# Kernel tuning notes

Hardware: AMD Instinct MI355X
Metric: run time of the kernel (lower is better)

## Reference

```python
import jax, jax.numpy as jnp
import numpy as np
from math import sqrt

NUM_HEADS = 8
HIDDEN = 768
ATTN_DIM = HIDDEN // NUM_HEADS  # 96
NEG = -1e10


def setup_inputs() -> dict:
    key = jax.random.key(0)
    ks = jax.random.split(key, 6)
    b, s, dim = 8, 1024, 768
    scale = 1.0 / sqrt(dim)
    return {
        "span_embeddings": jax.random.normal(ks[0], (b, s, dim), dtype=jnp.float32),
        "span_tags": jax.random.randint(ks[1], (b, s), 0, 5),
        "w_weight": jax.random.normal(ks[2], (1, dim), dtype=jnp.float32) * scale,
        "w_q": jax.random.normal(ks[3], (HIDDEN, dim), dtype=jnp.float32) * scale,
        "w_k": jax.random.normal(ks[4], (HIDDEN, dim), dtype=jnp.float32) * scale,
        "w_v": jax.random.normal(ks[5], (HIDDEN, dim), dtype=jnp.float32) * scale,
    }


def reference(span_embeddings, span_tags, w_weight, w_q, w_k, w_v):
    b, s, _ = span_embeddings.shape
    pad = span_tags == 0  # [b, s]

    # additive span attention weights: Linear(dim -> 1), mask padded, softmax over seq
    attn_weights = span_embeddings @ w_weight.T  # [b, s, 1]
    attn_weights = jnp.where(pad[:, :, None], NEG, attn_weights)
    attn_weights = jax.nn.softmax(attn_weights, axis=1)

    # NOTE: original views hidden as (attn_dim, num_heads) in that order
    qs = (span_embeddings @ w_q.T).reshape(b, s, ATTN_DIM, NUM_HEADS)
    ks = (span_embeddings @ w_k.T).reshape(b, s, ATTN_DIM, NUM_HEADS)
    vs = (span_embeddings @ w_v.T).reshape(b, s, ATTN_DIM, NUM_HEADS)

    rel = jnp.einsum('bqdh,bkdh->bqkh', qs, ks) / sqrt(ATTN_DIM)  # [b,q,k,h]
    # original masks along query axis (relevance_weights[span_tags.eq(0)] = NEG)
    rel = jnp.where(pad[:, :, None, None], NEG, rel)
    # original softmax(dim=-1) -> over the HEADS axis (faithful quirk)
    rel = jax.nn.softmax(rel, axis=-1)

    span_value = jnp.einsum('bqkh,bkdh->bqdh', rel, vs).reshape(b, s, HIDDEN)
    weighted_value = jnp.sum(attn_weights * span_value, axis=1)  # [b, hidden]
    return weighted_value
```

## Files before the change

kernel.cpp:

```cpp
#include <hip/hip_runtime.h>
#include <hip/hip_bf16.h>
#include <math.h>

#define NEGV (-1e10f)

typedef __attribute__((ext_vector_type(8))) short bf16x8;
typedef __attribute__((ext_vector_type(4))) float f32x4;
typedef __attribute__((ext_vector_type(16))) float f32x16;

static __device__ __forceinline__ unsigned short f2bf(float f) {
  unsigned int u = __builtin_bit_cast(unsigned int, f);
  unsigned int r = (u + 0x7fffu + ((u >> 16) & 1u)) >> 16;
  return (unsigned short)r;
}
static __device__ __forceinline__ float bf2f(unsigned short v) {
  return __builtin_bit_cast(float, (unsigned int)v << 16);
}

#define GLD16(g, l)                                                   \
  __builtin_amdgcn_global_load_lds(                                   \
      (const __attribute__((address_space(1))) void*)(g),             \
      (__attribute__((address_space(3))) void*)(l), 16, 0, 0)

__global__ __launch_bounds__(256) void cast_inputs(
    const float* __restrict__ emb, const int* __restrict__ tags,
    const float* __restrict__ ww, const float* __restrict__ wq,
    const float* __restrict__ wk, const float* __restrict__ wv,
    unsigned short* __restrict__ embbf, float* __restrict__ logits,
    unsigned short* __restrict__ wbf) {
  int bx = blockIdx.x;
  if (bx < 2048) {
    int w = threadIdx.x >> 6, lane = threadIdx.x & 63;
    int row = bx * 4 + w;
    const float4* src = (const float4*)(emb + (size_t)row * 768);
    const float4* wsrc = (const float4*)ww;
    ushort4* dst = (ushort4*)(embbf + (size_t)row * 768);
    float d = 0.f;
#pragma unroll
    for (int j = 0; j < 3; j++) {
      int idx = lane + 64 * j;
      float4 v = src[idx];
      float4 wv = wsrc[idx];
      d += v.x * wv.x + v.y * wv.y + v.z * wv.z + v.w * wv.w;
      ushort4 o;
      o.x = f2bf(v.x); o.y = f2bf(v.y); o.z = f2bf(v.z); o.w = f2bf(v.w);
      dst[idx] = o;
    }
#pragma unroll
    for (int off = 32; off; off >>= 1) d += __shfl_xor(d, off);
    if (lane == 0) logits[row] = (tags[row] == 0) ? NEGV : d;
  } else {
    int g = bx - 2048;
    int z = g / 576;
    int idx = (g - z * 576) * 256 + threadIdx.x;
    const float* src = (z == 0) ? wq : (z == 1) ? wk : wv;
    float4 v = ((const float4*)src)[idx];
    ushort4 o;
    o.x = f2bf(v.x); o.y = f2bf(v.y); o.z = f2bf(v.z); o.w = f2bf(v.w);
    ((ushort4*)(wbf + (size_t)z * 589824))[idx] = o;
  }
}

__global__ __launch_bounds__(256) void softmax_aw(
    const float* __restrict__ logits, float* __restrict__ aw) {
  __shared__ float red[4];
  int b = blockIdx.x, t = threadIdx.x;
  const float* L = logits + b * 1024;
  float x0 = L[t], x1 = L[t + 256], x2 = L[t + 512], x3 = L[t + 768];
  float m = fmaxf(fmaxf(x0, x1), fmaxf(x2, x3));
#pragma unroll
  for (int off = 32; off; off >>= 1) m = fmaxf(m, __shfl_xor(m, off));
  if ((t & 63) == 0) red[t >> 6] = m;
  __syncthreads();
  m = fmaxf(fmaxf(red[0], red[1]), fmaxf(red[2], red[3]));
  float e0 = __expf(x0 - m), e1 = __expf(x1 - m), e2 = __expf(x2 - m),
        e3 = __expf(x3 - m);
  float s = e0 + e1 + e2 + e3;
#pragma unroll
  for (int off = 32; off; off >>= 1) s += __shfl_xor(s, off);
  __syncthreads();
  if ((t & 63) == 0) red[t >> 6] = s;
  __syncthreads();
  float inv = 1.0f / (red[0] + red[1] + red[2] + red[3]);
  float* A = aw + b * 1024;
  A[t] = e0 * inv; A[t + 256] = e1 * inv;
  A[t + 512] = e2 * inv; A[t + 768] = e3 * inv;
}

__global__ __launch_bounds__(256) void qkv_gemm(
    const unsigned short* __restrict__ A, const unsigned short* __restrict__ Wbf,
    unsigned short* __restrict__ Qf, unsigned short* __restrict__ Kf,
    unsigned short* __restrict__ Vbf) {
  __shared__ __align__(16) unsigned short sm[16640];
  unsigned short* As = sm;
  unsigned short* Bs = sm + 8192;
  int z = blockIdx.z;
  const unsigned short* B = Wbf + (size_t)z * 589824;
  int mb = blockIdx.x * 128, nb = blockIdx.y * 128;
  int tid = threadIdx.x;
  int w = tid >> 6, lane = tid & 63;
  int wm = w >> 1, wn = w & 1;
  int c = lane & 15, quad = lane >> 4;
  int lrow = lane >> 2;
  int lcol = ((lane & 3) ^ (lrow & 3)) * 8;
  const unsigned short* Ag = A + (size_t)(mb + w * 32 + lrow) * 768 + lcol;
  const unsigned short* Bg = B + (size_t)(nb + w * 32 + lrow) * 768 + lcol;
  int woff = w * 1024;

#define PREFETCH(buf, kb)                                              \
  do {                                                                 \
    GLD16(Ag + (kb), As + (buf) * 4096 + woff);                        \
    GLD16(Ag + (kb) + 16 * 768, As + (buf) * 4096 + woff + 512);       \
    GLD16(Bg + (kb), Bs + (buf) * 4096 + woff);                        \
    GLD16(Bg + (kb) + 16 * 768, Bs + (buf) * 4096 + woff + 512);       \
  } while (0)

  f32x4 acc[4][4];
#pragma unroll
  for (int i = 0; i < 4; i++)
#pragma unroll
    for (int j = 0; j < 4; j++) acc[i][j] = 0;

  PREFETCH(0, 0);
  for (int it = 0; it < 24; it++) {
    __syncthreads();
    if (it + 1 < 24) PREFETCH((it + 1) & 1, (it + 1) * 32);
    const unsigned short* Ab = As + (it & 1) * 4096;
    const unsigned short* Bb = Bs + (it & 1) * 4096;
    int sw = (quad ^ (c & 3)) * 8;
    bf16x8 af[4], bfr[4];
#pragma unroll
    for (int i = 0; i < 4; i++)
      af[i] = *(const bf16x8*)&Ab[(wm * 64 + i * 16 + c) * 32 + sw];
#pragma unroll
    for (int j = 0; j < 4; j++)
      bfr[j] = *(const bf16x8*)&Bb[(wn * 64 + j * 16 + c) * 32 + sw];
#pragma unroll
    for (int i = 0; i < 4; i++)
#pragma unroll
      for (int j = 0; j < 4; j++)
        acc[i][j] = __builtin_amdgcn_mfma_f32_16x16x32_bf16(af[i], bfr[j],
                                                            acc[i][j], 0, 0, 0);
  }
  __syncthreads();

  if (z == 2) {
#pragma unroll
    for (int i = 0; i < 4; i++)
#pragma unroll
      for (int j = 0; j < 4; j++)
#pragma unroll
        for (int r = 0; r < 4; r++) {
          int rowg = mb + wm * 64 + i * 16 + quad * 4 + r;
          int colg = nb + wn * 64 + j * 16 + c;
          Vbf[(size_t)rowg * 768 + colg] = f2bf(acc[i][j][r]);
        }
  } else {
    unsigned short* O = (z == 0) ? Qf : Kf;
#pragma unroll
    for (int i = 0; i < 4; i++) {
#pragma unroll
      for (int j = 0; j < 4; j++) {
#pragma unroll
        for (int r = 0; r < 4; r++) {
          int ql = wm * 64 + i * 16 + quad * 4 + r;
          int h = c & 7;
          int elem = j * 2 + (c >> 3);
          int chunkL = (ql >> 5) * 8 + h;
          int lane32 = (ql & 31) + wn * 32;
          sm[chunkL * 520 + lane32 * 8 + elem] = f2bf(acc[i][j][r]);
        }
      }
    }
    __syncthreads();
    int bq = mb >> 10;
    int qt32g0 = (mb & 1023) >> 5;
    int tt = blockIdx.y;
#pragma unroll
    for (int it2 = 0; it2 < 8; it2++) {
      int g = it2 * 256 + tid;
      int chunkL = g >> 6;
      int off = (g & 63) * 8;
      bf16x8 vdat = *(const bf16x8*)&sm[chunkL * 520 + off];
      int qt32 = qt32g0 + (chunkL >> 3), h = chunkL & 7;
      size_t dst = ((((size_t)(bq * 32 + qt32) * 8 + h) * 6 + tt) << 9) + off;
      *(bf16x8*)&O[dst] = vdat;
    }
  }
#undef PREFETCH
}

__global__ __launch_bounds__(256) void attn(
    const unsigned short* __restrict__ Qf, const unsigned short* __restrict__ Kf,
    const float* __restrict__ aw, float* __restrict__ Ptp) {
  __shared__ float pbuf[1024];
  int b = blockIdx.z, qb = blockIdx.y, kb = blockIdx.x;
  int tid = threadIdx.x, w = tid >> 6, lane = tid & 63;
  int wq = w >> 1, wk = w & 1;
  const unsigned short* Qb =
      Qf + ((size_t)(b * 32 + qb * 2 + wq) * 48) * 512 + (size_t)lane * 8;
  const unsigned short* Kb =
      Kf + ((size_t)(b * 32 + kb * 2 + wk) * 48) * 512 + (size_t)lane * 8;

  f32x16 acc[8];
#pragma unroll
  for (int h = 0; h < 8; h++) acc[h] = 0;
#pragma unroll
  for (int h = 0; h < 8; h++) {
#pragma unroll
    for (int t = 0; t < 6; t++) {
      bf16x8 a = *(const bf16x8*)(Qb + (size_t)(h * 6 + t) * 512);
      bf16x8 bb = *(const bf16x8*)(Kb + (size_t)(h * 6 + t) * 512);
      acc[h] = __builtin_amdgcn_mfma_f32_32x32x16_bf16(a, bb, acc[h], 0, 0, 0);
    }
  }

  float awv[16];
#pragma unroll
  for (int reg = 0; reg < 16; reg++) {
    int row = (reg & 3) + 8 * (reg >> 2) + 4 * (lane >> 5);
    awv[reg] = aw[b * 1024 + qb * 64 + wq * 32 + row];
  }
  float partial[8];
#pragma unroll
  for (int h = 0; h < 8; h++) partial[h] = 0.f;
  const float C2 = 0.10206207261596577f * 1.4426950408889634f;
#pragma unroll
  for (int reg = 0; reg < 16; reg++) {
    float v[8];
    float ssum = 0.f;
#pragma unroll
    for (int h = 0; h < 8; h++) {
      float e = exp2f(acc[h][reg] * C2);
      v[h] = e;
      ssum += e;
    }
    float g = awv[reg] * __builtin_amdgcn_rcpf(ssum);
#pragma unroll
    for (int h = 0; h < 8; h++) partial[h] += v[h] * g;
  }
#pragma unroll
  for (int h = 0; h < 8; h++) {
    float v = partial[h];
    v += __shfl_xor(v, 32);
    partial[h] = v;
  }
  if (lane < 32) {
#pragma unroll
    for (int h = 0; h < 8; h++) pbuf[w * 256 + lane * 8 + h] = partial[h];
  }
  __syncthreads();
#pragma unroll
  for (int wk2 = 0; wk2 < 2; wk2++) {
    float s = pbuf[wk2 * 256 + tid] + pbuf[(2 + wk2) * 256 + tid];
    int kcol = tid >> 3, h = tid & 7;
    Ptp[(((size_t)qb * 8 + b) * 1024 + kb * 64 + wk2 * 32 + kcol) * 8 + h] = s;
  }
}

__global__ __launch_bounds__(256) void finalize(
    const float* __restrict__ Ptp, const unsigned short* __restrict__ Vbf,
    float* __restrict__ out) {
  __shared__ float ps[256];
  int kc = blockIdx.x, b = blockIdx.y;
  int t = threadIdx.x;
  {
    int k = kc * 32 + (t >> 3), h = t & 7;
    float s = 0.f;
#pragma unroll
    for (int qc = 0; qc < 16; qc++)
      s += Ptp[(((size_t)qc * 8 + b) * 1024 + k) * 8 + h];
    ps[t] = s;
  }
  __syncthreads();
  if (t < 192) {
    int o0 = t * 4;
    int hb = o0 & 7;
    float a0 = 0, a1 = 0, a2 = 0, a3 = 0;
    const unsigned short* Vb = Vbf + ((size_t)b * 1024 + kc * 32) * 768 + o0;
#pragma unroll 4
    for (int kk = 0; kk < 32; kk++) {
      ushort4 vv = *(const ushort4*)(Vb + (size_t)kk * 768);
      const float* p = &ps[kk * 8 + hb];
      a0 += p[0] * bf2f(vv.x);
      a1 += p[1] * bf2f(vv.y);
      a2 += p[2] * bf2f(vv.z);
      a3 += p[3] * bf2f(vv.w);
    }
    atomicAdd(&out[b * 768 + o0], a0);
    atomicAdd(&out[b * 768 + o0 + 1], a1);
    atomicAdd(&out[b * 768 + o0 + 2], a2);
    atomicAdd(&out[b * 768 + o0 + 3], a3);
  }
}

extern "C" void kernel_launch(void* const* d_in, const int* in_sizes, int n_in,
                              void* d_out, int out_size, void* d_ws,
                              size_t ws_size, hipStream_t stream) {
  const float* emb = (const float*)d_in[0];
  const int* tags = (const int*)d_in[1];
  const float* ww = (const float*)d_in[2];
  const float* wq = (const float*)d_in[3];
  const float* wk = (const float*)d_in[4];
  const float* wv = (const float*)d_in[5];
  float* out = (float*)d_out;
  char* ws = (char*)d_ws;
  unsigned short* embbf = (unsigned short*)(ws + 0);
  unsigned short* wbf   = (unsigned short*)(ws + 12582912);
  unsigned short* Qf    = (unsigned short*)(ws + 16121856);
  unsigned short* Kf    = (unsigned short*)(ws + 28704768);
  unsigned short* Vbf   = (unsigned short*)(ws + 41287680);
  float* logits         = (float*)(ws + 53870592);
  float* aw             = (float*)(ws + 53903360);
  float* Ptp            = (float*)(ws + 53936128);

  hipMemsetAsync(out, 0, 8 * 768 * sizeof(float), stream);
  cast_inputs<<<3776, 256, 0, stream>>>(emb, tags, ww, wq, wk, wv, embbf,
                                        logits, wbf);
  softmax_aw<<<8, 256, 0, stream>>>(logits, aw);
  qkv_gemm<<<dim3(64, 6, 3), 256, 0, stream>>>(embbf, wbf, Qf, Kf, Vbf);
  attn<<<dim3(16, 16, 8), 256, 0, stream>>>(Qf, Kf, aw, Ptp);
  finalize<<<dim3(32, 8), 256, 0, stream>>>(Ptp, Vbf, out);
}
```

Baseline: 171.6 us.

## Stage Q tiles in LDS for larger attn blocks and coalesce QKV GEMM stores

The attn kernel now runs 512-thread blocks that each cover 128 keys. The 64-query Q tile is loaded once into LDS with global_load_lds and shared by all 8 waves, which halves the grid and cuts redundant Q global reads. The W_q/W_k rows are permuted during the cast, so the GEMM epilogue can write packed ushort4 values into shared memory for Q and K. V is now staged through shared memory before being written out as 16-byte coalesced stores. In exchange, LDS use per block rises to about 104KB and the extra syncs may lower occupancy.

```diff
diff --git a/kernel.cpp b/kernel.cpp
--- a/kernel.cpp
+++ b/kernel.cpp
@@ -57,7 +57,17 @@
     float4 v = ((const float4*)src)[idx];
     ushort4 o;
     o.x = f2bf(v.x); o.y = f2bf(v.y); o.z = f2bf(v.z); o.w = f2bf(v.w);
-    ((ushort4*)(wbf + (size_t)z * 589824))[idx] = o;
+    if (z == 2) {
+      ((ushort4*)(wbf + (size_t)z * 589824))[idx] = o;
+    } else {
+      int f = idx / 192;
+      int col4 = idx - f * 192;
+      int h = f & 7, dg = f >> 3;
+      int tt = dg >> 4, ddl = dg & 15;
+      int wn = ddl >> 3, cb = (ddl >> 2) & 1, j = ddl & 3;
+      int orow = tt * 128 + wn * 64 + j * 16 + cb * 8 + h;
+      ((ushort4*)(wbf + (size_t)z * 589824))[orow * 192 + col4] = o;
+    }
   }
 }
 
@@ -91,7 +101,7 @@
     const unsigned short* __restrict__ A, const unsigned short* __restrict__ Wbf,
     unsigned short* __restrict__ Qf, unsigned short* __restrict__ Kf,
     unsigned short* __restrict__ Vbf) {
-  __shared__ __align__(16) unsigned short sm[16640];
+  __shared__ __align__(16) unsigned short sm[17408];
   unsigned short* As = sm;
   unsigned short* Bs = sm + 8192;
   int z = blockIdx.z;
@@ -151,25 +161,34 @@
       for (int j = 0; j < 4; j++)
 #pragma unroll
         for (int r = 0; r < 4; r++) {
-          int rowg = mb + wm * 64 + i * 16 + quad * 4 + r;
-          int colg = nb + wn * 64 + j * 16 + c;
-          Vbf[(size_t)rowg * 768 + colg] = f2bf(acc[i][j][r]);
+          int rl = wm * 64 + i * 16 + quad * 4 + r;
+          int cl = wn * 64 + j * 16 + c;
+          sm[rl * 136 + cl] = f2bf(acc[i][j][r]);
         }
+    __syncthreads();
+#pragma unroll
+    for (int it2 = 0; it2 < 8; it2++) {
+      int g2 = it2 * 256 + tid;
+      int rl = g2 >> 4;
+      int cu = (g2 & 15) * 8;
+      bf16x8 vdat = *(const bf16x8*)&sm[rl * 136 + cu];
+      *(bf16x8*)&Vbf[(size_t)(mb + rl) * 768 + nb + cu] = vdat;
+    }
   } else {
     unsigned short* O = (z == 0) ? Qf : Kf;
 #pragma unroll
     for (int i = 0; i < 4; i++) {
 #pragma unroll
-      for (int j = 0; j < 4; j++) {
-#pragma unroll
-        for (int r = 0; r < 4; r++) {
-          int ql = wm * 64 + i * 16 + quad * 4 + r;
-          int h = c & 7;
-          int elem = j * 2 + (c >> 3);
-          int chunkL = (ql >> 5) * 8 + h;
-          int lane32 = (ql & 31) + wn * 32;
-          sm[chunkL * 520 + lane32 * 8 + elem] = f2bf(acc[i][j][r]);
-        }
+      for (int r = 0; r < 4; r++) {
+        int qlr = wm * 64 + i * 16 + quad * 4 + r;
+        int chunkL = (qlr >> 5) * 8 + (c & 7);
+        int lane32 = (qlr & 31) + wn * 32;
+        ushort4 pk;
+        pk.x = f2bf(acc[i][0][r]);
+        pk.y = f2bf(acc[i][1][r]);
+        pk.z = f2bf(acc[i][2][r]);
+        pk.w = f2bf(acc[i][3][r]);
+        *(ushort4*)&sm[chunkL * 520 + lane32 * 8 + 4 * (c >> 3)] = pk;
       }
     }
     __syncthreads();
@@ -190,17 +209,28 @@
 #undef PREFETCH
 }
 
-__global__ __launch_bounds__(256) void attn(
+__global__ __launch_bounds__(512) void attn(
     const unsigned short* __restrict__ Qf, const unsigned short* __restrict__ Kf,
     const float* __restrict__ aw, float* __restrict__ Ptp) {
-  __shared__ float pbuf[1024];
+  __shared__ __align__(16) unsigned short Qs[49152];
+  __shared__ float pbuf[2048];
   int b = blockIdx.z, qb = blockIdx.y, kb = blockIdx.x;
   int tid = threadIdx.x, w = tid >> 6, lane = tid & 63;
-  int wq = w >> 1, wk = w & 1;
-  const unsigned short* Qb =
-      Qf + ((size_t)(b * 32 + qb * 2 + wq) * 48) * 512 + (size_t)lane * 8;
-  const unsigned short* Kb =
-      Kf + ((size_t)(b * 32 + kb * 2 + wk) * 48) * 512 + (size_t)lane * 8;
+  int wq2 = w >> 2, wk2 = w & 3;
+
+#pragma unroll
+  for (int call = 0; call < 12; call++) {
+    int cc = call * 8 + w;
+    int q32 = cc / 48, rem = cc - q32 * 48;
+    size_t src =
+        ((size_t)((b * 32 + qb * 2 + q32) * 48 + rem) << 9) + (size_t)lane * 8;
+    GLD16(Qf + src, Qs + cc * 512);
+  }
+  __syncthreads();
+
+  const unsigned short* Kc =
+      Kf + ((size_t)(b * 32 + kb * 4 + wk2) * 48 << 9) + (size_t)lane * 8;
+  const unsigned short* Qw = Qs + wq2 * 48 * 512 + (size_t)lane * 8;
 
   f32x16 acc[8];
 #pragma unroll
@@ -209,8 +239,8 @@
   for (int h = 0; h < 8; h++) {
 #pragma unroll
     for (int t = 0; t < 6; t++) {
-      bf16x8 a = *(const bf16x8*)(Qb + (size_t)(h * 6 + t) * 512);
-      bf16x8 bb = *(const bf16x8*)(Kb + (size_t)(h * 6 + t) * 512);
+      bf16x8 a = *(const bf16x8*)(Qw + (size_t)(h * 6 + t) * 512);
+      bf16x8 bb = *(const bf16x8*)(Kc + (size_t)(h * 6 + t) * 512);
       acc[h] = __builtin_amdgcn_mfma_f32_32x32x16_bf16(a, bb, acc[h], 0, 0, 0);
     }
   }
@@ -219,7 +249,7 @@
 #pragma unroll
   for (int reg = 0; reg < 16; reg++) {
     int row = (reg & 3) + 8 * (reg >> 2) + 4 * (lane >> 5);
-    awv[reg] = aw[b * 1024 + qb * 64 + wq * 32 + row];
+    awv[reg] = aw[b * 1024 + qb * 64 + wq2 * 32 + row];
   }
   float partial[8];
 #pragma unroll
@@ -251,10 +281,12 @@
   }
   __syncthreads();
 #pragma unroll
-  for (int wk2 = 0; wk2 < 2; wk2++) {
-    float s = pbuf[wk2 * 256 + tid] + pbuf[(2 + wk2) * 256 + tid];
-    int kcol = tid >> 3, h = tid & 7;
-    Ptp[(((size_t)qb * 8 + b) * 1024 + kb * 64 + wk2 * 32 + kcol) * 8 + h] = s;
+  for (int half = 0; half < 2; half++) {
+    int idx = half * 512 + tid;
+    int wko = idx >> 8, rem2 = idx & 255;
+    float s = pbuf[wko * 256 + rem2] + pbuf[(wko + 4) * 256 + rem2];
+    int kcol = rem2 >> 3, h = rem2 & 7;
+    Ptp[(((size_t)qb * 8 + b) * 1024 + kb * 128 + wko * 32 + kcol) * 8 + h] = s;
   }
 }
 
@@ -319,6 +351,6 @@
                                         logits, wbf);
   softmax_aw<<<8, 256, 0, stream>>>(logits, aw);
   qkv_gemm<<<dim3(64, 6, 3), 256, 0, stream>>>(embbf, wbf, Qf, Kf, Vbf);
-  attn<<<dim3(16, 16, 8), 256, 0, stream>>>(Qf, Kf, aw, Ptp);
+  attn<<<dim3(8, 16, 8), 512, 0, stream>>>(Qf, Kf, aw, Ptp);
   finalize<<<dim3(32, 8), 256, 0, stream>>>(Ptp, Vbf, out);
 }
```

Measured after the change: 186.7 us. +8.8%, slower.
